# Kernel tuning notes

Measured on AMD Instinct MI355X. Metric: run time of the kernel, lower is better.

## Reference

```python
import jax, jax.numpy as jnp
import numpy as np

B, T, S, C, H = 2, 2048, 2048, 1024, 16
D = C // H  # head dim = 64


def setup_inputs() -> dict:
    key = jax.random.key(0)
    ks = jax.random.split(key, 6)
    sc = 1.0 / np.sqrt(C)
    return {
        "q": jax.random.normal(ks[0], (B, T, C), jnp.float32),
        "p": jax.random.normal(ks[1], (B, S, C), jnp.float32),
        "Wq": jax.random.normal(ks[2], (C, C), jnp.float32) * sc,
        "Wk": jax.random.normal(ks[3], (C, C), jnp.float32) * sc,
        "Wv": jax.random.normal(ks[4], (C, C), jnp.float32) * sc,
        "Wo": jax.random.normal(ks[5], (C, C), jnp.float32) * sc,
    }


def reference(q, p, Wq, Wk, Wv, Wo):
    # Linear projections (no bias: config.bias=True -> nn.Linear bias=False)
    qh = (q @ Wq).reshape(B, T, H, D)  # [B,T,H,D]
    kh = (p @ Wk).reshape(B, S, H, D)  # [B,S,H,D]
    vh = (p @ Wv).reshape(B, S, H, D)  # [B,S,H,D]
    scale = 1.0 / jnp.sqrt(jnp.asarray(D, qh.dtype))
    att = jnp.einsum('bthd,bshd->bhts', qh, kh) * scale  # [B,H,T,S]
    att = jax.nn.softmax(att, axis=-1)
    y = jnp.einsum('bhts,bshd->bthd', att, vh).reshape(B, T, C)
    y = y @ Wo  # c_proj, dropout p=0 (eval)
    return y
```

## Files before the change

kernel.cpp:

```cpp
#include <hip/hip_runtime.h>
#include <hip/hip_bf16.h>
#include <stdint.h>

#define T_LEN 2048
#define CDIM  1024

typedef short bf16x8_t  __attribute__((ext_vector_type(8)));
typedef float f32x4_t   __attribute__((ext_vector_type(4)));
typedef float f32x16_t  __attribute__((ext_vector_type(16)));

__device__ __forceinline__ float fexp2(float x) {
  float r;
  asm("v_exp_f32 %0, %1" : "=v"(r) : "v"(x));
  return r;
}

__device__ __forceinline__ void gload_lds16(const void* gptr, void* lptr) {
  __builtin_amdgcn_global_load_lds(
      (const __attribute__((address_space(1))) unsigned int*)(gptr),
      (__attribute__((address_space(3))) unsigned int*)(lptr),
      16, 0, 0);
}

__device__ __forceinline__ void wait_vm0_barrier() {
  asm volatile("s_waitcnt vmcnt(0)" ::: "memory");
  __builtin_amdgcn_sched_barrier(0);
  __builtin_amdgcn_s_barrier();
  __builtin_amdgcn_sched_barrier(0);
}

__device__ __forceinline__ unsigned short f2bf(float f) {
  union { float f; unsigned int u; } v; v.f = f;
  unsigned int u = v.u;
  return (unsigned short)((u + 0x7fffu + ((u >> 16) & 1u)) >> 16);
}

__device__ __forceinline__ unsigned int pk_bf16(float lo, float hi) {
  unsigned int r;
  asm("v_cvt_pk_bf16_f32 %0, %1, %2" : "=v"(r) : "v"(lo), "v"(hi));
  return r;
}
__device__ __forceinline__ unsigned short bf1(float v) {
  return (unsigned short)pk_bf16(v, v);
}
__device__ __forceinline__ float bf2f(unsigned short u) {
  union { unsigned int u; float f; } v; v.u = ((unsigned int)u) << 16;
  return v.f;
}

__global__ __launch_bounds__(256) void cast2_f32_bf16(const float* __restrict__ x0,
                                                      const float* __restrict__ x1,
                                                      unsigned short* __restrict__ y0,
                                                      unsigned short* __restrict__ y1) {
  int i = blockIdx.x * 256 + threadIdx.x;
  const float* x = blockIdx.y ? x1 : x0;
  unsigned short* y = blockIdx.y ? y1 : y0;
  const float4* x4 = (const float4*)x;
  float4 a = x4[i * 2], b = x4[i * 2 + 1];
  union { unsigned short u[8]; uint4 v; } o;
  o.u[0] = f2bf(a.x); o.u[1] = f2bf(a.y); o.u[2] = f2bf(a.z); o.u[3] = f2bf(a.w);
  o.u[4] = f2bf(b.x); o.u[5] = f2bf(b.y); o.u[6] = f2bf(b.z); o.u[7] = f2bf(b.w);
  ((uint4*)y)[i] = o.v;
}

__global__ __launch_bounds__(256) void transpose_cast4(const float* __restrict__ W0,
                                                       const float* __restrict__ W1,
                                                       const float* __restrict__ W2,
                                                       const float* __restrict__ W3,
                                                       unsigned short* __restrict__ Wall,
                                                       unsigned short* __restrict__ Wot) {
  __shared__ float tile[32][33];
  int z = blockIdx.z;
  const float* W = (z == 0) ? W0 : (z == 1) ? W1 : (z == 2) ? W2 : W3;
  unsigned short* Wt = (z < 3) ? (Wall + (size_t)z * 1024 * 1024) : Wot;
  int tx = threadIdx.x & 31, ty = threadIdx.x >> 5;
  int n0 = blockIdx.x * 32, k0 = blockIdx.y * 32;
#pragma unroll
  for (int i = 0; i < 4; ++i) {
    int r = ty + i * 8;
    tile[r][tx] = W[(size_t)(k0 + r) * CDIM + n0 + tx];
  }
  __syncthreads();
#pragma unroll
  for (int i = 0; i < 4; ++i) {
    int r = ty + i * 8;
    Wt[(size_t)(n0 + r) * CDIM + k0 + tx] = f2bf(tile[tx][r]);
  }
}

__global__ __launch_bounds__(256) void gemm_qkv(const unsigned short* __restrict__ qbm,
                                                const unsigned short* __restrict__ pbm,
                                                const unsigned short* __restrict__ Wall,
                                                unsigned short* __restrict__ Qh,
                                                unsigned short* __restrict__ Kh,
                                                unsigned short* __restrict__ Vt) {
  __shared__ unsigned short ldsA[2][128 * 64];
  __shared__ unsigned short ldsB[2][64 * 64];
  const int tid = threadIdx.x, lane = tid & 63, w = tid >> 6;
  const int bid = blockIdx.x;
  const int xcd = bid & 7, local = bid >> 3;
  const int pm = xcd & 3, pn = xcd >> 2;
  const int lm = local & 7, ln = local >> 3;
  const int mblk = pm * 8 + lm;
  const int nblk = pn * 24 + ln;
  const int m0 = mblk * 128;
  const int n0 = nblk * 64;
  const char* Ab = (const char*)((nblk < 16) ? qbm : pbm);
  const char* Bb = (const char*)Wall;
  f32x4_t acc[2][4] = {};

  auto stage = [&](int buf, int kt) {
#pragma unroll
    for (int it = 0; it < 4; ++it) {
      int ob = it * 4096 + w * 1024;
      int o = ob + lane * 16;
      int row = o >> 7, cin = o & 127;
      int cs = cin ^ ((row & 7) << 4);
      gload_lds16(Ab + (size_t)(m0 + row) * 2048 + kt * 128 + cs, (char*)ldsA[buf] + ob);
    }
#pragma unroll
    for (int it = 0; it < 2; ++it) {
      int ob = it * 4096 + w * 1024;
      int o = ob + lane * 16;
      int row = o >> 7, cin = o & 127;
      int cs = cin ^ ((row & 7) << 4);
      gload_lds16(Bb + (size_t)(n0 + row) * 2048 + kt * 128 + cs, (char*)ldsB[buf] + ob);
    }
  };

  stage(0, 0);
  wait_vm0_barrier();
  stage(1, 1);
  for (int kt = 0; kt < 16; ++kt) {
    const char* lA = (const char*)ldsA[kt & 1];
    const char* lB = (const char*)ldsB[kt & 1];
#pragma unroll
    for (int kf = 0; kf < 2; ++kf) {
      int c = kf * 64 + ((lane >> 4) << 4);
      bf16x8_t af[2], bfr[4];
#pragma unroll
      for (int mf = 0; mf < 2; ++mf) {
        int row = w * 32 + mf * 16 + (lane & 15);
        af[mf] = *(const bf16x8_t*)(lA + row * 128 + (c ^ ((row & 7) << 4)));
      }
#pragma unroll
      for (int nf = 0; nf < 4; ++nf) {
        int row = nf * 16 + (lane & 15);
        bfr[nf] = *(const bf16x8_t*)(lB + row * 128 + (c ^ ((row & 7) << 4)));
      }
#pragma unroll
      for (int mf = 0; mf < 2; ++mf)
#pragma unroll
        for (int nf = 0; nf < 4; ++nf)
          acc[mf][nf] = __builtin_amdgcn_mfma_f32_16x16x32_bf16(af[mf], bfr[nf], acc[mf][nf], 0, 0, 0);
    }
    if (kt < 15) {
      wait_vm0_barrier();
      if (kt + 2 < 16) stage(kt & 1, kt + 2);
    }
  }

  const float oscale = (nblk < 16) ? 0.18033688011112042f : 1.0f;
#pragma unroll
  for (int mf = 0; mf < 2; ++mf)
#pragma unroll
    for (int nf = 0; nf < 4; ++nf)
#pragma unroll
      for (int j = 0; j < 4; ++j) {
        int row = m0 + w * 32 + mf * 16 + ((lane >> 4) << 2) + j;
        int col = n0 + nf * 16 + (lane & 15);
        float v = acc[mf][nf][j] * oscale;
        int b = row >> 11, ts = row & 2047;
        if (col < 1024) {
          int h = col >> 6, d = col & 63;
          Qh[(((size_t)(b * 16 + h)) * 2048 + ts) * 64 + d] = bf1(v);
        } else if (col < 2048) {
          int cc = col - 1024, h = cc >> 6, d = cc & 63;
          Kh[(((size_t)(b * 16 + h)) * 2048 + ts) * 64 + d] = bf1(v);
        } else {
          int cc = col - 2048, h = cc >> 6, d = cc & 63;
          Vt[(((size_t)(b * 16 + h)) * 64 + d) * 2048 + ts] = bf1(v);
        }
      }
}

__global__ __launch_bounds__(256) void gemm_out(const unsigned short* __restrict__ A,
                                                const unsigned short* __restrict__ Bt,
                                                float* __restrict__ Out) {
  __shared__ unsigned short ldsA[2][128 * 64];
  __shared__ unsigned short ldsB[2][64 * 64];
  const int tid = threadIdx.x, lane = tid & 63, w = tid >> 6;
  const int bid = blockIdx.x;
  const int xcd = bid & 7, local = bid >> 3;
  const int pm = xcd & 3, pn = xcd >> 2;
  const int lm = local & 7, ln = local >> 3;
  const int m0 = (pm * 8 + lm) * 128;
  const int n0 = (pn * 8 + ln) * 64;
  const char* Ab = (const char*)A;
  const char* Bb = (const char*)Bt;
  f32x4_t acc[2][4] = {};

  auto stage = [&](int buf, int kt) {
#pragma unroll
    for (int it = 0; it < 4; ++it) {
      int ob = it * 4096 + w * 1024;
      int o = ob + lane * 16;
      int row = o >> 7, cin = o & 127;
      int cs = cin ^ ((row & 7) << 4);
      gload_lds16(Ab + (size_t)(m0 + row) * 2048 + kt * 128 + cs, (char*)ldsA[buf] + ob);
    }
#pragma unroll
    for (int it = 0; it < 2; ++it) {
      int ob = it * 4096 + w * 1024;
      int o = ob + lane * 16;
      int row = o >> 7, cin = o & 127;
      int cs = cin ^ ((row & 7) << 4);
      gload_lds16(Bb + (size_t)(n0 + row) * 2048 + kt * 128 + cs, (char*)ldsB[buf] + ob);
    }
  };

  stage(0, 0);
  wait_vm0_barrier();
  stage(1, 1);
  for (int kt = 0; kt < 16; ++kt) {
    const char* lA = (const char*)ldsA[kt & 1];
    const char* lB = (const char*)ldsB[kt & 1];
#pragma unroll
    for (int kf = 0; kf < 2; ++kf) {
      int c = kf * 64 + ((lane >> 4) << 4);
      bf16x8_t af[2], bfr[4];
#pragma unroll
      for (int mf = 0; mf < 2; ++mf) {
        int row = w * 32 + mf * 16 + (lane & 15);
        af[mf] = *(const bf16x8_t*)(lA + row * 128 + (c ^ ((row & 7) << 4)));
      }
#pragma unroll
      for (int nf = 0; nf < 4; ++nf) {
        int row = nf * 16 + (lane & 15);
        bfr[nf] = *(const bf16x8_t*)(lB + row * 128 + (c ^ ((row & 7) << 4)));
      }
#pragma unroll
      for (int mf = 0; mf < 2; ++mf)
#pragma unroll
        for (int nf = 0; nf < 4; ++nf)
          acc[mf][nf] = __builtin_amdgcn_mfma_f32_16x16x32_bf16(af[mf], bfr[nf], acc[mf][nf], 0, 0, 0);
    }
    if (kt < 15) {
      wait_vm0_barrier();
      if (kt + 2 < 16) stage(kt & 1, kt + 2);
    }
  }

#pragma unroll
  for (int mf = 0; mf < 2; ++mf)
#pragma unroll
    for (int nf = 0; nf < 4; ++nf)
#pragma unroll
      for (int j = 0; j < 4; ++j) {
        int row = m0 + w * 32 + mf * 16 + ((lane >> 4) << 2) + j;
        int col = n0 + nf * 16 + (lane & 15);
        Out[(size_t)row * 1024 + col] = acc[mf][nf][j];
      }
}

template <int SPLIT>
__global__ __launch_bounds__(256, 3) void attn32(const unsigned short* __restrict__ Qg,
                                                 const unsigned short* __restrict__ Kg,
                                                 const unsigned short* __restrict__ Vtg,
                                                 unsigned short* __restrict__ Ag,
                                                 unsigned short* __restrict__ OpA,
                                                 unsigned short* __restrict__ OpB,
                                                 float* __restrict__ Lp) {
  __shared__ unsigned short ldsK[3][64 * 64];
  __shared__ unsigned short ldsV[2][64 * 64];
  const int tid = threadIdx.x, lane = tid & 63, w = tid >> 6;
  const int hi = lane >> 5, ql = lane & 31;
  const int bid = blockIdx.x;
  int bh, z, qtile;
  if (SPLIT == 2) {
    int comb = bid & 63;
    qtile = bid >> 6;
    bh = comb >> 1;
    z = comb & 1;
  } else {
    bh = bid & 31;
    qtile = bid >> 5;
    z = 0;
  }
  const int q0 = qtile * 128 + w * 32;
  constexpr int NT = 2048 / SPLIT / 64;
  const int sBeg = z * (2048 / SPLIT);

  bf16x8_t qf[4];
#pragma unroll
  for (int kd = 0; kd < 4; ++kd)
    qf[kd] = *(const bf16x8_t*)(Qg + ((size_t)bh * T_LEN + q0 + ql) * 64 + kd * 16 + hi * 8);

  bf16x8_t ones;
#pragma unroll
  for (int i = 0; i < 8; ++i) ones[i] = (short)0x3F80;

  f32x16_t oacc[2] = {};
  f32x16_t lacc = {};
  const f32x16_t vzero = {};

  const char* Kb = (const char*)(Kg + (size_t)bh * 2048 * 64);
  const char* Vb = (const char*)(Vtg + (size_t)bh * 64 * 2048);

  auto stageK = [&](int slot, int t) {
    int s0 = sBeg + t * 64;
#pragma unroll
    for (int it = 0; it < 2; ++it) {
      int ob = it * 4096 + w * 1024;
      int o = ob + lane * 16;
      int row = o >> 7, cin = o & 127;
      int cs = cin ^ ((row & 7) << 4);
      gload_lds16(Kb + (size_t)s0 * 128 + row * 128 + cs, (char*)ldsK[slot] + ob);
    }
  };
  auto stageV = [&](int slot, int t) {
    int s0 = sBeg + t * 64;
#pragma unroll
    for (int it = 0; it < 2; ++it) {
      int ob = it * 4096 + w * 1024;
      int o = ob + lane * 16;
      int row = o >> 7, cin = o & 127;
      int cs = cin ^ ((row & 7) << 4);
      gload_lds16(Vb + (size_t)s0 * 2 + (size_t)row * 4096 + cs, (char*)ldsV[slot] + ob);
    }
  };

  auto qk = [&](f32x16_t (&s)[2], int slot) {
    const char* lK = (const char*)ldsK[slot];
#pragma unroll
    for (int sub = 0; sub < 2; ++sub) {
      int row = sub * 32 + ql;
      int swz = (row & 7) << 4;
#pragma unroll
      for (int kd = 0; kd < 4; ++kd) {
        bf16x8_t kfrag = *(const bf16x8_t*)(lK + row * 128 + ((kd * 32 + hi * 16) ^ swz));
        s[sub] = __builtin_amdgcn_mfma_f32_32x32x16_bf16(kfrag, qf[kd], s[sub], 0, 0, 0);
      }
    }
  };

  auto consume = [&](f32x16_t (&s)[2], int vslot) {
    const char* lV = (const char*)ldsV[vslot];
#pragma unroll
    for (int ks = 0; ks < 4; ++ks) {
      const int sub = ks >> 1, mA = (ks & 1) * 2, mB = mA + 1;
      float e0 = fexp2(s[sub][4 * mA + 0]), e1 = fexp2(s[sub][4 * mA + 1]);
      float e2 = fexp2(s[sub][4 * mA + 2]), e3 = fexp2(s[sub][4 * mA + 3]);
      float e4 = fexp2(s[sub][4 * mB + 0]), e5 = fexp2(s[sub][4 * mB + 1]);
      float e6 = fexp2(s[sub][4 * mB + 2]), e7 = fexp2(s[sub][4 * mB + 3]);
      unsigned int a0 = pk_bf16(e0, e1), a1 = pk_bf16(e2, e3);
      unsigned int b0 = pk_bf16(e4, e5), b1 = pk_bf16(e6, e7);
      asm("v_permlane32_swap_b32 %0, %1" : "+v"(a0), "+v"(b0));
      asm("v_permlane32_swap_b32 %0, %1" : "+v"(a1), "+v"(b1));
      union { unsigned int u[4]; bf16x8_t v; } P;
      P.u[0] = a0; P.u[1] = a1; P.u[2] = b0; P.u[3] = b1;
      lacc = __builtin_amdgcn_mfma_f32_32x32x16_bf16(P.v, ones, lacc, 0, 0, 0);
#pragma unroll
      for (int dt = 0; dt < 2; ++dt) {
        int row = dt * 32 + ql;
        bf16x8_t vfrag = *(const bf16x8_t*)(lV + row * 128 + ((ks * 32 + hi * 16) ^ ((row & 7) << 4)));
        oacc[dt] = __builtin_amdgcn_mfma_f32_32x32x16_bf16(P.v, vfrag, oacc[dt], 0, 0, 0);
      }
    }
  };

  f32x16_t sA[2] = {}, sB[2] = {};
  stageK(0, 0);
  stageV(0, 0);
  stageK(1, 1);
  __syncthreads();
  qk(sA, 0);

  for (int i = 0; i < NT; i += 2) {
    if (i + 2 < NT) stageK((i + 2) % 3, i + 2);
    if (i + 1 < NT) stageV((i + 1) & 1, i + 1);
    if (i + 1 < NT) { sB[0] = vzero; sB[1] = vzero; qk(sB, (i + 1) % 3); }
    consume(sA, i & 1);
    __syncthreads();
    if (i + 1 < NT) {
      if (i + 3 < NT) stageK((i + 3) % 3, i + 3);
      if (i + 2 < NT) stageV((i + 2) & 1, i + 2);
      if (i + 2 < NT) { sA[0] = vzero; sA[1] = vzero; qk(sA, (i + 2) % 3); }
      consume(sB, (i + 1) & 1);
      __syncthreads();
    }
  }

  const int b = bh >> 4, h = bh & 15;
  if (SPLIT == 1) {
#pragma unroll
    for (int grp = 0; grp < 4; ++grp)
#pragma unroll
      for (int r2 = 0; r2 < 4; ++r2) {
        int reg = grp * 4 + r2;
        float linv = 1.0f / lacc[reg];
        int t = q0 + 4 * hi + 8 * grp + r2;
#pragma unroll
        for (int dt = 0; dt < 2; ++dt) {
          int col = h * 64 + dt * 32 + ql;
          float v = oacc[dt][reg] * linv;
          Ag[((size_t)b * T_LEN + t) * CDIM + col] = bf1(v);
        }
      }
  } else {
    unsigned short* Op = z ? OpB : OpA;
#pragma unroll
    for (int grp = 0; grp < 4; ++grp)
#pragma unroll
      for (int r2 = 0; r2 < 4; ++r2) {
        int reg = grp * 4 + r2;
        int t = q0 + 4 * hi + 8 * grp + r2;
#pragma unroll
        for (int dt = 0; dt < 2; ++dt)
          Op[((size_t)b * T_LEN + t) * CDIM + h * 64 + dt * 32 + ql] = bf1(oacc[dt][reg]);
        if (ql == 0)
          Lp[(((size_t)z * 2 + b) * 16 + h) * T_LEN + t] = lacc[reg];
      }
  }
}

__global__ __launch_bounds__(256) void attn_combine(const unsigned short* __restrict__ O0,
                                                    const unsigned short* __restrict__ O1,
                                                    const float* __restrict__ Lp,
                                                    unsigned short* __restrict__ Ag) {
  int i = blockIdx.x * 256 + threadIdx.x;
  int c8 = i & 127, bt = i >> 7;
  int b = bt >> 11, t = bt & 2047;
  int c = c8 * 8, h = c >> 6;
  float l0 = Lp[(((size_t)0 * 2 + b) * 16 + h) * T_LEN + t];
  float l1 = Lp[(((size_t)1 * 2 + b) * 16 + h) * T_LEN + t];
  float inv = 1.0f / (l0 + l1);
  size_t off = (size_t)bt * CDIM + c;
  union { unsigned short u[8]; uint4 v; } a, bb, o;
  a.v  = *(const uint4*)(O0 + off);
  bb.v = *(const uint4*)(O1 + off);
  float s[8];
#pragma unroll
  for (int k = 0; k < 8; ++k) s[k] = (bf2f(a.u[k]) + bf2f(bb.u[k])) * inv;
  unsigned int p0 = pk_bf16(s[0], s[1]), p1 = pk_bf16(s[2], s[3]);
  unsigned int p2 = pk_bf16(s[4], s[5]), p3 = pk_bf16(s[6], s[7]);
  o.v = make_uint4(p0, p1, p2, p3);
  *(uint4*)(Ag + off) = o.v;
}

extern "C" void kernel_launch(void* const* d_in, const int* in_sizes, int n_in,
                              void* d_out, int out_size, void* d_ws, size_t ws_size,
                              hipStream_t stream) {
  const float* q  = (const float*)d_in[0];
  const float* p  = (const float*)d_in[1];
  const float* Wq = (const float*)d_in[2];
  const float* Wk = (const float*)d_in[3];
  const float* Wv = (const float*)d_in[4];
  const float* Wo = (const float*)d_in[5];

  char* ws = (char*)d_ws;
  const size_t MB = (size_t)1 << 20;
  unsigned short* qb   = (unsigned short*)(ws);
  unsigned short* pb   = (unsigned short*)(ws + 8 * MB);
  unsigned short* Wall = (unsigned short*)(ws + 16 * MB);
  unsigned short* Wot  = (unsigned short*)(ws + 22 * MB);
  unsigned short* Qh   = (unsigned short*)(ws + 24 * MB);
  unsigned short* Kh   = (unsigned short*)(ws + 32 * MB);
  unsigned short* Vt   = (unsigned short*)(ws + 40 * MB);
  unsigned short* Ao   = (unsigned short*)(ws + 48 * MB);

  cast2_f32_bf16<<<dim3(2048, 2), 256, 0, stream>>>(q, p, qb, pb);
  transpose_cast4<<<dim3(32, 32, 4), 256, 0, stream>>>(Wq, Wk, Wv, Wo, Wall, Wot);

  gemm_qkv<<<1536, 256, 0, stream>>>(qb, pb, Wall, Qh, Kh, Vt);

  if (ws_size >= 73 * MB) {
    unsigned short* O0 = (unsigned short*)(ws);
    unsigned short* O1 = (unsigned short*)(ws + 56 * MB);
    float* Lp = (float*)(ws + 72 * MB);
    attn32<2><<<1024, 256, 0, stream>>>(Qh, Kh, Vt, nullptr, O0, O1, Lp);
    attn_combine<<<2048, 256, 0, stream>>>(O0, O1, Lp, Ao);
  } else {
    attn32<1><<<512, 256, 0, stream>>>(Qh, Kh, Vt, Ao, nullptr, nullptr, nullptr);
  }

  gemm_out<<<512, 256, 0, stream>>>(Ao, Wot, (float*)d_out);
}
```

Before: 130.0 us.

## Enlarge QKV GEMM tile to 128x128 and switch to 32x32x16 MFMA

The QKV projection GEMM tile grows from 128x64 to 128x128, which halves the grid to 768 blocks. Each wave now computes a 64x64 sub-tile with 32x32x16 bf16 MFMAs in place of 16x16x32. The goal is more arithmetic per LDS and global load, with fewer B-operand re-reads across blocks. In exchange it uses more LDS and accumulator registers, which may lower occupancy, and the smaller grid may fill the CUs less evenly.

```diff
diff --git a/kernel.cpp b/kernel.cpp
--- a/kernel.cpp
+++ b/kernel.cpp
@@ -95,19 +95,21 @@
                                                 unsigned short* __restrict__ Kh,
                                                 unsigned short* __restrict__ Vt) {
   __shared__ unsigned short ldsA[2][128 * 64];
-  __shared__ unsigned short ldsB[2][64 * 64];
+  __shared__ unsigned short ldsB[2][128 * 64];
   const int tid = threadIdx.x, lane = tid & 63, w = tid >> 6;
+  const int wr = w >> 1, wc = w & 1;
+  const int hi = lane >> 5, ql = lane & 31;
   const int bid = blockIdx.x;
   const int xcd = bid & 7, local = bid >> 3;
   const int pm = xcd & 3, pn = xcd >> 2;
   const int lm = local & 7, ln = local >> 3;
   const int mblk = pm * 8 + lm;
-  const int nblk = pn * 24 + ln;
+  const int nblk = pn * 12 + ln;
   const int m0 = mblk * 128;
-  const int n0 = nblk * 64;
-  const char* Ab = (const char*)((nblk < 16) ? qbm : pbm);
+  const int n0 = nblk * 128;
+  const char* Ab = (const char*)((nblk < 8) ? qbm : pbm);
   const char* Bb = (const char*)Wall;
-  f32x4_t acc[2][4] = {};
+  f32x16_t acc[2][2] = {};
 
   auto stage = [&](int buf, int kt) {
 #pragma unroll
@@ -117,13 +119,6 @@
       int row = o >> 7, cin = o & 127;
       int cs = cin ^ ((row & 7) << 4);
       gload_lds16(Ab + (size_t)(m0 + row) * 2048 + kt * 128 + cs, (char*)ldsA[buf] + ob);
-    }
-#pragma unroll
-    for (int it = 0; it < 2; ++it) {
-      int ob = it * 4096 + w * 1024;
-      int o = ob + lane * 16;
-      int row = o >> 7, cin = o & 127;
-      int cs = cin ^ ((row & 7) << 4);
       gload_lds16(Bb + (size_t)(n0 + row) * 2048 + kt * 128 + cs, (char*)ldsB[buf] + ob);
     }
   };
@@ -135,24 +130,24 @@
     const char* lA = (const char*)ldsA[kt & 1];
     const char* lB = (const char*)ldsB[kt & 1];
 #pragma unroll
-    for (int kf = 0; kf < 2; ++kf) {
-      int c = kf * 64 + ((lane >> 4) << 4);
-      bf16x8_t af[2], bfr[4];
-#pragma unroll
-      for (int mf = 0; mf < 2; ++mf) {
-        int row = w * 32 + mf * 16 + (lane & 15);
-        af[mf] = *(const bf16x8_t*)(lA + row * 128 + (c ^ ((row & 7) << 4)));
-      }
-#pragma unroll
-      for (int nf = 0; nf < 4; ++nf) {
-        int row = nf * 16 + (lane & 15);
-        bfr[nf] = *(const bf16x8_t*)(lB + row * 128 + (c ^ ((row & 7) << 4)));
-      }
-#pragma unroll
-      for (int mf = 0; mf < 2; ++mf)
-#pragma unroll
-        for (int nf = 0; nf < 4; ++nf)
-          acc[mf][nf] = __builtin_amdgcn_mfma_f32_16x16x32_bf16(af[mf], bfr[nf], acc[mf][nf], 0, 0, 0);
+    for (int kf = 0; kf < 4; ++kf) {
+      int cb = kf * 32 + hi * 16;
+      bf16x8_t af[2], bfr[2];
+#pragma unroll
+      for (int s = 0; s < 2; ++s) {
+        int row = wr * 64 + s * 32 + ql;
+        af[s] = *(const bf16x8_t*)(lA + row * 128 + (cb ^ ((row & 7) << 4)));
+      }
+#pragma unroll
+      for (int t = 0; t < 2; ++t) {
+        int row = wc * 64 + t * 32 + ql;
+        bfr[t] = *(const bf16x8_t*)(lB + row * 128 + (cb ^ ((row & 7) << 4)));
+      }
+#pragma unroll
+      for (int s = 0; s < 2; ++s)
+#pragma unroll
+        for (int t = 0; t < 2; ++t)
+          acc[s][t] = __builtin_amdgcn_mfma_f32_32x32x16_bf16(af[s], bfr[t], acc[s][t], 0, 0, 0);
     }
     if (kt < 15) {
       wait_vm0_barrier();
@@ -160,16 +155,16 @@
     }
   }
 
-  const float oscale = (nblk < 16) ? 0.18033688011112042f : 1.0f;
-#pragma unroll
-  for (int mf = 0; mf < 2; ++mf)
-#pragma unroll
-    for (int nf = 0; nf < 4; ++nf)
-#pragma unroll
-      for (int j = 0; j < 4; ++j) {
-        int row = m0 + w * 32 + mf * 16 + ((lane >> 4) << 2) + j;
-        int col = n0 + nf * 16 + (lane & 15);
-        float v = acc[mf][nf][j] * oscale;
+  const float oscale = (nblk < 8) ? 0.18033688011112042f : 1.0f;
+#pragma unroll
+  for (int s = 0; s < 2; ++s)
+#pragma unroll
+    for (int t = 0; t < 2; ++t)
+#pragma unroll
+      for (int reg = 0; reg < 16; ++reg) {
+        int row = m0 + wr * 64 + s * 32 + (reg & 3) + 8 * (reg >> 2) + 4 * hi;
+        int col = n0 + wc * 64 + t * 32 + ql;
+        float v = acc[s][t][reg] * oscale;
         int b = row >> 11, ts = row & 2047;
         if (col < 1024) {
           int h = col >> 6, d = col & 63;
@@ -472,7 +467,7 @@
   cast2_f32_bf16<<<dim3(2048, 2), 256, 0, stream>>>(q, p, qb, pb);
   transpose_cast4<<<dim3(32, 32, 4), 256, 0, stream>>>(Wq, Wk, Wv, Wo, Wall, Wot);
 
-  gemm_qkv<<<1536, 256, 0, stream>>>(qb, pb, Wall, Qh, Kh, Vt);
+  gemm_qkv<<<768, 256, 0, stream>>>(qb, pb, Wall, Qh, Kh, Vt);
 
   if (ws_size >= 73 * MB) {
     unsigned short* O0 = (unsigned short*)(ws);
```

After: 138.5 us. 6.5% more time.

## Fuse split-KV attention combine into output projection GEMM A-tile loading

Applied to the files above, without the earlier changes.

Removes the separate attn_combine kernel and performs the two-partial sum and normalization while staging A tiles inside gemm_out. A tiles are loaded into registers, combined with the per-row softmax denominators (head index equals k-tile), converted to bf16 and written to swizzled LDS. This saves one launch and a full write-and-reread of the combined activation buffer. In exchange, A staging goes through registers rather than direct global-to-LDS loads and reads twice the A bytes, which may reduce latency hiding in the GEMM loop.

```diff
diff --git a/kernel.cpp b/kernel.cpp
--- a/kernel.cpp
+++ b/kernel.cpp
@@ -24,6 +24,12 @@
 
 __device__ __forceinline__ void wait_vm0_barrier() {
   asm volatile("s_waitcnt vmcnt(0)" ::: "memory");
+  __builtin_amdgcn_sched_barrier(0);
+  __builtin_amdgcn_s_barrier();
+  __builtin_amdgcn_sched_barrier(0);
+}
+__device__ __forceinline__ void wait_lgkm0_barrier() {
+  asm volatile("s_waitcnt lgkmcnt(0)" ::: "memory");
   __builtin_amdgcn_sched_barrier(0);
   __builtin_amdgcn_s_barrier();
   __builtin_amdgcn_sched_barrier(0);
@@ -184,7 +190,10 @@
       }
 }
 
-__global__ __launch_bounds__(256) void gemm_out(const unsigned short* __restrict__ A,
+template <int FUSE>
+__global__ __launch_bounds__(256) void gemm_out(const unsigned short* __restrict__ A0,
+                                                const unsigned short* __restrict__ A1,
+                                                const float* __restrict__ Lp,
                                                 const unsigned short* __restrict__ Bt,
                                                 float* __restrict__ Out) {
   __shared__ unsigned short ldsA[2][128 * 64];
@@ -196,32 +205,80 @@
   const int lm = local & 7, ln = local >> 3;
   const int m0 = (pm * 8 + lm) * 128;
   const int n0 = (pn * 8 + ln) * 64;
-  const char* Ab = (const char*)A;
   const char* Bb = (const char*)Bt;
   f32x4_t acc[2][4] = {};
 
-  auto stage = [&](int buf, int kt) {
+  auto stageB = [&](int buf, int kt) {
+#pragma unroll
+    for (int it = 0; it < 2; ++it) {
+      int ob = it * 4096 + w * 1024;
+      int o = ob + lane * 16;
+      int row = o >> 7, cin = o & 127;
+      int cs = cin ^ ((row & 7) << 4);
+      gload_lds16(Bb + (size_t)(n0 + row) * 2048 + kt * 128 + cs, (char*)ldsB[buf] + ob);
+    }
+  };
+  auto stageA_lds = [&](int buf, int kt) {
 #pragma unroll
     for (int it = 0; it < 4; ++it) {
       int ob = it * 4096 + w * 1024;
       int o = ob + lane * 16;
       int row = o >> 7, cin = o & 127;
       int cs = cin ^ ((row & 7) << 4);
-      gload_lds16(Ab + (size_t)(m0 + row) * 2048 + kt * 128 + cs, (char*)ldsA[buf] + ob);
-    }
-#pragma unroll
-    for (int it = 0; it < 2; ++it) {
-      int ob = it * 4096 + w * 1024;
-      int o = ob + lane * 16;
-      int row = o >> 7, cin = o & 127;
-      int cs = cin ^ ((row & 7) << 4);
-      gload_lds16(Bb + (size_t)(n0 + row) * 2048 + kt * 128 + cs, (char*)ldsB[buf] + ob);
-    }
-  };
-
-  stage(0, 0);
-  wait_vm0_barrier();
-  stage(1, 1);
+      gload_lds16((const char*)A0 + (size_t)(m0 + row) * 2048 + kt * 128 + cs, (char*)ldsA[buf] + ob);
+    }
+  };
+
+  uint4 ra[4], rb[4];
+  float rl0[4], rl1[4];
+  auto issueA = [&](int kt) {
+#pragma unroll
+    for (int it = 0; it < 4; ++it) {
+      int cc = w * 4 + it;
+      int o = cc * 1024 + lane * 16;
+      int row = o >> 7, cin = o & 127;
+      int m = m0 + row, b = m >> 11, t = m & 2047;
+      size_t abyte = (size_t)m * 2048 + kt * 128 + cin;
+      ra[it] = *(const uint4*)((const char*)A0 + abyte);
+      rb[it] = *(const uint4*)((const char*)A1 + abyte);
+      rl0[it] = Lp[(((size_t)0 * 2 + b) * 16 + kt) * T_LEN + t];
+      rl1[it] = Lp[(((size_t)1 * 2 + b) * 16 + kt) * T_LEN + t];
+    }
+  };
+  auto writeA = [&](int buf) {
+#pragma unroll
+    for (int it = 0; it < 4; ++it) {
+      int cc = w * 4 + it;
+      int o = cc * 1024 + lane * 16;
+      int row = o >> 7, cin = o & 127;
+      float inv = 1.0f / (rl0[it] + rl1[it]);
+      union { unsigned short u[8]; uint4 v; } a, b, ov;
+      a.v = ra[it]; b.v = rb[it];
+      float s[8];
+#pragma unroll
+      for (int k = 0; k < 8; ++k) s[k] = (bf2f(a.u[k]) + bf2f(b.u[k])) * inv;
+      ov.v = make_uint4(pk_bf16(s[0], s[1]), pk_bf16(s[2], s[3]),
+                        pk_bf16(s[4], s[5]), pk_bf16(s[6], s[7]));
+      *(uint4*)((char*)ldsA[buf] + row * 128 + (cin ^ ((row & 7) << 4))) = ov.v;
+    }
+  };
+
+  if (FUSE) {
+    issueA(0);
+    stageB(0, 0);
+    asm volatile("s_waitcnt vmcnt(0)" ::: "memory");
+    writeA(0);
+    issueA(1);
+    stageB(1, 1);
+    wait_lgkm0_barrier();
+  } else {
+    stageA_lds(0, 0);
+    stageB(0, 0);
+    wait_vm0_barrier();
+    stageA_lds(1, 1);
+    stageB(1, 1);
+  }
+
   for (int kt = 0; kt < 16; ++kt) {
     const char* lA = (const char*)ldsA[kt & 1];
     const char* lB = (const char*)ldsB[kt & 1];
@@ -246,8 +303,15 @@
           acc[mf][nf] = __builtin_amdgcn_mfma_f32_16x16x32_bf16(af[mf], bfr[nf], acc[mf][nf], 0, 0, 0);
     }
     if (kt < 15) {
-      wait_vm0_barrier();
-      if (kt + 2 < 16) stage(kt & 1, kt + 2);
+      if (FUSE) {
+        asm volatile("s_waitcnt vmcnt(0)" ::: "memory");
+        writeA((kt + 1) & 1);
+        wait_lgkm0_barrier();
+        if (kt + 2 < 16) { issueA(kt + 2); stageB(kt & 1, kt + 2); }
+      } else {
+        wait_vm0_barrier();
+        if (kt + 2 < 16) { stageA_lds(kt & 1, kt + 2); stageB(kt & 1, kt + 2); }
+      }
     }
   }
 
@@ -424,30 +488,6 @@
   }
 }
 
-__global__ __launch_bounds__(256) void attn_combine(const unsigned short* __restrict__ O0,
-                                                    const unsigned short* __restrict__ O1,
-                                                    const float* __restrict__ Lp,
-                                                    unsigned short* __restrict__ Ag) {
-  int i = blockIdx.x * 256 + threadIdx.x;
-  int c8 = i & 127, bt = i >> 7;
-  int b = bt >> 11, t = bt & 2047;
-  int c = c8 * 8, h = c >> 6;
-  float l0 = Lp[(((size_t)0 * 2 + b) * 16 + h) * T_LEN + t];
-  float l1 = Lp[(((size_t)1 * 2 + b) * 16 + h) * T_LEN + t];
-  float inv = 1.0f / (l0 + l1);
-  size_t off = (size_t)bt * CDIM + c;
-  union { unsigned short u[8]; uint4 v; } a, bb, o;
-  a.v  = *(const uint4*)(O0 + off);
-  bb.v = *(const uint4*)(O1 + off);
-  float s[8];
-#pragma unroll
-  for (int k = 0; k < 8; ++k) s[k] = (bf2f(a.u[k]) + bf2f(bb.u[k])) * inv;
-  unsigned int p0 = pk_bf16(s[0], s[1]), p1 = pk_bf16(s[2], s[3]);
-  unsigned int p2 = pk_bf16(s[4], s[5]), p3 = pk_bf16(s[6], s[7]);
-  o.v = make_uint4(p0, p1, p2, p3);
-  *(uint4*)(Ag + off) = o.v;
-}
-
 extern "C" void kernel_launch(void* const* d_in, const int* in_sizes, int n_in,
                               void* d_out, int out_size, void* d_ws, size_t ws_size,
                               hipStream_t stream) {
@@ -479,10 +519,9 @@
     unsigned short* O1 = (unsigned short*)(ws + 56 * MB);
     float* Lp = (float*)(ws + 72 * MB);
     attn32<2><<<1024, 256, 0, stream>>>(Qh, Kh, Vt, nullptr, O0, O1, Lp);
-    attn_combine<<<2048, 256, 0, stream>>>(O0, O1, Lp, Ao);
+    gemm_out<1><<<512, 256, 0, stream>>>(O0, O1, Lp, Wot, (float*)d_out);
   } else {
     attn32<1><<<512, 256, 0, stream>>>(Qh, Kh, Vt, Ao, nullptr, nullptr, nullptr);
-  }
-
-  gemm_out<<<512, 256, 0, stream>>>(Ao, Wot, (float*)d_out);
-}
+    gemm_out<0><<<512, 256, 0, stream>>>(Ao, nullptr, nullptr, Wot, (float*)d_out);
+  }
+}
```

Result: slower. 135.3 us (+4.1%).
